# Optimization experiments

Hardware: AMD Instinct MI355X
Metric: run time of the kernel (lower is better)

Reference implementation:

```python
import jax, jax.numpy as jnp
import numpy as np

NUM_GRAPHS = 128
HIDDEN = 256
EPS = 1e-8


def setup_inputs() -> dict:
    key = jax.random.key(0)
    k1, k2, k3, k4, k5, k6, k7 = jax.random.split(key, 7)
    N = 100000
    node_feat = jax.random.normal(k1, (N, HIDDEN), dtype=jnp.float32)
    node_pos = jax.random.normal(k2, (N, 3), dtype=jnp.float32)
    batch = jnp.sort(jax.random.randint(k3, (N,), 0, NUM_GRAPHS))
    # mlp_node_feat: Linear(1, hidden) -> SiLU -> Linear(hidden, hidden)
    W1 = jax.random.normal(k4, (1, HIDDEN), dtype=jnp.float32) * (1.0 / np.sqrt(1.0))
    b1 = jax.random.normal(k5, (HIDDEN,), dtype=jnp.float32) * 0.01
    W2 = jax.random.normal(k6, (HIDDEN, HIDDEN), dtype=jnp.float32) * (1.0 / np.sqrt(HIDDEN))
    b2 = jax.random.normal(k7, (HIDDEN,), dtype=jnp.float32) * 0.01
    return {"node_feat": node_feat, "node_pos": node_pos, "batch": batch,
            "W1": W1, "b1": b1, "W2": W2, "b2": b2}


def _scatter_mean(x, seg, num_segments):
    # sum per segment / count (empty segments -> 0, matching nan_to_num)
    sums = jax.ops.segment_sum(x, seg, num_segments=num_segments)
    counts = jax.ops.segment_sum(jnp.ones((x.shape[0], 1), x.dtype), seg,
                                 num_segments=num_segments)
    return jnp.where(counts > 0, sums / jnp.maximum(counts, 1.0), 0.0)


def reference(node_feat, node_pos, batch, W1, b1, W2, b2):
    # center of each graph, gathered back to nodes
    center = _scatter_mean(node_pos, batch, NUM_GRAPHS)          # [G, 3]
    pos = node_pos - center[batch]                               # [N, 3]
    # safe_norm with keepdim
    scalar = jnp.maximum(jnp.linalg.norm(pos, axis=1, keepdims=True), EPS)  # [N, 1]
    # mlp_node_feat: Linear -> SiLU -> Linear
    h = jax.nn.silu(scalar @ W1 + b1)                            # [N, H]
    return h @ W2 + b2                                           # [N, H]
```

## Files before the change

kernel.cpp:

```cpp
#include <hip/hip_runtime.h>
#include <math.h>

#define HIDDEN   256
#define G_NUM    128
#define TN       1024
#define DS       (1.0f/64.0f)
#define INV_DS   64.0f
#define TM       4
#define TBLOCKS  (TN/TM)
#define CBLOCKS  G_NUM
#define LGRID    2048

typedef float f32x4 __attribute__((ext_vector_type(4)));

__device__ __forceinline__ float readlane_f(float v, int l) {
    union { float f; unsigned u; } a, r;
    a.f = v;
    r.u = __builtin_amdgcn_readlane(a.u, l);
    return r.f;
}

__device__ __forceinline__ float silu_f(float x) {
    return x / (1.f + __expf(-x));
}

__global__ __launch_bounds__(256)
void prep_kernel(const float* __restrict__ pos,
                 const int*   __restrict__ batch,
                 const float* __restrict__ W1,
                 const float* __restrict__ b1,
                 const float* __restrict__ W2,
                 const float* __restrict__ b2,
                 int N,
                 float* __restrict__ U,
                 float* __restrict__ T)
{
    const int bid = blockIdx.x;
    const int tid = threadIdx.x;

    if (bid < TBLOCKS) {
        int k  = tid;
        int l  = tid & 63;
        int m0 = bid * TM;
        float s0 = (float)(m0 + 0) * DS;
        float s1 = (float)(m0 + 1) * DS;
        float s2 = (float)(m0 + 2) * DS;
        float s3 = (float)(m0 + 3) * DS;
        float a0 = 0.f, a1 = 0.f, a2 = 0.f, a3 = 0.f;

        for (int c = 0; c < HIDDEN / 64; ++c) {
            int jb = c * 64;
            float w1 = W1[jb + l];
            float bb = b1[jb + l];
            float h0 = silu_f(fmaf(s0, w1, bb));
            float h1 = silu_f(fmaf(s1, w1, bb));
            float h2 = silu_f(fmaf(s2, w1, bb));
            float h3 = silu_f(fmaf(s3, w1, bb));
            const float* w2p = W2 + (size_t)jb * HIDDEN + k;
            #pragma unroll
            for (int jj = 0; jj < 64; ++jj) {
                float w = w2p[(size_t)jj * HIDDEN];
                a0 = fmaf(readlane_f(h0, jj), w, a0);
                a1 = fmaf(readlane_f(h1, jj), w, a1);
                a2 = fmaf(readlane_f(h2, jj), w, a2);
                a3 = fmaf(readlane_f(h3, jj), w, a3);
            }
        }
        float bv = b2[k];
        T[(size_t)(m0 + 0) * HIDDEN + k] = a0 + bv;
        T[(size_t)(m0 + 1) * HIDDEN + k] = a1 + bv;
        T[(size_t)(m0 + 2) * HIDDEN + k] = a2 + bv;
        T[(size_t)(m0 + 3) * HIDDEN + k] = a3 + bv;
        return;
    }

    int g = bid - TBLOCKS;

    int lo0 = 0, hi0 = N, lo1 = 0, hi1 = N;
    while (lo0 < hi0 || lo1 < hi1) {
        if (lo0 < hi0) { int m = (lo0 + hi0) >> 1; if (batch[m] <  g) lo0 = m + 1; else hi0 = m; }
        if (lo1 < hi1) { int m = (lo1 + hi1) >> 1; if (batch[m] <= g) lo1 = m + 1; else hi1 = m; }
    }
    int start = lo0, end = lo1;
    int cnt = end - start;
    if (cnt <= 0) return;

    float sx = 0.f, sy = 0.f, sz = 0.f;
    for (int n = start + tid; n < end; n += 256) {
        sx += pos[n * 3 + 0];
        sy += pos[n * 3 + 1];
        sz += pos[n * 3 + 2];
    }
    #pragma unroll
    for (int m = 32; m > 0; m >>= 1) {
        sx += __shfl_xor(sx, m, 64);
        sy += __shfl_xor(sy, m, 64);
        sz += __shfl_xor(sz, m, 64);
    }
    __shared__ float cw[3][4];
    __shared__ float ctr[3];
    int w    = tid >> 6;
    int lane = tid & 63;
    if (lane == 0) { cw[0][w] = sx; cw[1][w] = sy; cw[2][w] = sz; }
    __syncthreads();
    if (tid == 0) {
        float inv = 1.f / (float)cnt;
        ctr[0] = (cw[0][0] + cw[0][1] + cw[0][2] + cw[0][3]) * inv;
        ctr[1] = (cw[1][0] + cw[1][1] + cw[1][2] + cw[1][3]) * inv;
        ctr[2] = (cw[2][0] + cw[2][1] + cw[2][2] + cw[2][3]) * inv;
    }
    __syncthreads();
    float cx = ctr[0], cy = ctr[1], cz = ctr[2];

    for (int n = start + tid; n < end; n += 256) {
        float dx = pos[n * 3 + 0] - cx;
        float dy = pos[n * 3 + 1] - cy;
        float dz = pos[n * 3 + 2] - cz;
        float s  = fmaxf(sqrtf(fmaf(dx, dx, fmaf(dy, dy, dz * dz))), 1e-8f);
        U[n] = s * INV_DS;
    }
}

__global__ __launch_bounds__(256)
void lerp_kernel(const float* __restrict__ U,
                 const float* __restrict__ T,
                 float* __restrict__ out, int N)
{
    const int w      = (blockIdx.x << 2) | (threadIdx.x >> 6);
    const int l      = threadIdx.x & 63;
    const int stride = LGRID * 4;

    const f32x4* T4   = (const f32x4*)T;
    f32x4*       out4 = (f32x4*)out;

    int n = w;
    for (; n + stride < N; n += 2 * stride) {
        int n1 = n + stride;
        float u0 = U[n];
        float u1 = U[n1];
        int   i0 = (int)u0; i0 = (i0 < TN - 2) ? i0 : (TN - 2);
        int   i1 = (int)u1; i1 = (i1 < TN - 2) ? i1 : (TN - 2);
        float f0 = u0 - (float)i0;
        float f1 = u1 - (float)i1;
        f32x4 A0 = T4[(size_t)i0       * (HIDDEN / 4) + l];
        f32x4 B0 = T4[(size_t)(i0 + 1) * (HIDDEN / 4) + l];
        f32x4 A1 = T4[(size_t)i1       * (HIDDEN / 4) + l];
        f32x4 B1 = T4[(size_t)(i1 + 1) * (HIDDEN / 4) + l];
        f32x4 o0, o1;
        o0.x = fmaf(f0, B0.x - A0.x, A0.x);
        o0.y = fmaf(f0, B0.y - A0.y, A0.y);
        o0.z = fmaf(f0, B0.z - A0.z, A0.z);
        o0.w = fmaf(f0, B0.w - A0.w, A0.w);
        o1.x = fmaf(f1, B1.x - A1.x, A1.x);
        o1.y = fmaf(f1, B1.y - A1.y, A1.y);
        o1.z = fmaf(f1, B1.z - A1.z, A1.z);
        o1.w = fmaf(f1, B1.w - A1.w, A1.w);
        __builtin_nontemporal_store(o0, &out4[(size_t)n  * (HIDDEN / 4) + l]);
        __builtin_nontemporal_store(o1, &out4[(size_t)n1 * (HIDDEN / 4) + l]);
    }
    for (; n < N; n += stride) {
        float u0 = U[n];
        int   i0 = (int)u0; i0 = (i0 < TN - 2) ? i0 : (TN - 2);
        float f0 = u0 - (float)i0;
        f32x4 A0 = T4[(size_t)i0       * (HIDDEN / 4) + l];
        f32x4 B0 = T4[(size_t)(i0 + 1) * (HIDDEN / 4) + l];
        f32x4 o0;
        o0.x = fmaf(f0, B0.x - A0.x, A0.x);
        o0.y = fmaf(f0, B0.y - A0.y, A0.y);
        o0.z = fmaf(f0, B0.z - A0.z, A0.z);
        o0.w = fmaf(f0, B0.w - A0.w, A0.w);
        __builtin_nontemporal_store(o0, &out4[(size_t)n * (HIDDEN / 4) + l]);
    }
}

extern "C" void kernel_launch(void* const* d_in, const int* in_sizes, int n_in,
                              void* d_out, int out_size, void* d_ws, size_t ws_size,
                              hipStream_t stream) {
    const float* node_pos = (const float*)d_in[1];
    const int*   batch    = (const int*)  d_in[2];
    const float* W1       = (const float*)d_in[3];
    const float* b1       = (const float*)d_in[4];
    const float* W2       = (const float*)d_in[5];
    const float* b2       = (const float*)d_in[6];
    float*       out      = (float*)d_out;

    int N = in_sizes[1] / 3;

    char*  ws = (char*)d_ws;
    float* U  = (float*)ws;
    float* T  = (float*)(ws + (512 << 10));

    prep_kernel<<<TBLOCKS + CBLOCKS, 256, 0, stream>>>(node_pos, batch,
                                                       W1, b1, W2, b2, N, U, T);
    lerp_kernel<<<LGRID, 256, 0, stream>>>(U, T, out, N);
}
```

Measured before the change: 32.02 us.

## Fuse centering and norm into lerp kernel, compute segment bounds by boundary detection

Segment bounds are now found by parallel boundary detection across many blocks instead of a per-graph binary search. The center computation and per-node norm move into the lerp kernel: each of 16 slices per graph recomputes the graph's center and then looks up the table directly. This drops the U intermediate array and its write/read round-trip. The cost is that the center reduction runs 16 times per graph, and load balance now depends on graph sizes.

```diff
diff --git a/kernel.cpp b/kernel.cpp
--- a/kernel.cpp
+++ b/kernel.cpp
@@ -8,8 +8,8 @@
 #define INV_DS   64.0f
 #define TM       4
 #define TBLOCKS  (TN/TM)
-#define CBLOCKS  G_NUM
-#define LGRID    2048
+#define SLICES   16
+#define LGRID    (G_NUM*SLICES)
 
 typedef float f32x4 __attribute__((ext_vector_type(4)));
 
@@ -25,15 +25,14 @@
 }
 
 __global__ __launch_bounds__(256)
-void prep_kernel(const float* __restrict__ pos,
-                 const int*   __restrict__ batch,
-                 const float* __restrict__ W1,
-                 const float* __restrict__ b1,
-                 const float* __restrict__ W2,
-                 const float* __restrict__ b2,
-                 int N,
-                 float* __restrict__ U,
-                 float* __restrict__ T)
+void table_bounds_kernel(const float* __restrict__ W1,
+                         const float* __restrict__ b1,
+                         const float* __restrict__ W2,
+                         const float* __restrict__ b2,
+                         const int*   __restrict__ batch,
+                         int N,
+                         int* __restrict__ bnd0, int* __restrict__ bnd1,
+                         float* __restrict__ T)
 {
     const int bid = blockIdx.x;
     const int tid = threadIdx.x;
@@ -71,18 +70,36 @@
         T[(size_t)(m0 + 1) * HIDDEN + k] = a1 + bv;
         T[(size_t)(m0 + 2) * HIDDEN + k] = a2 + bv;
         T[(size_t)(m0 + 3) * HIDDEN + k] = a3 + bv;
-        return;
-    }
-
-    int g = bid - TBLOCKS;
-
-    int lo0 = 0, hi0 = N, lo1 = 0, hi1 = N;
-    while (lo0 < hi0 || lo1 < hi1) {
-        if (lo0 < hi0) { int m = (lo0 + hi0) >> 1; if (batch[m] <  g) lo0 = m + 1; else hi0 = m; }
-        if (lo1 < hi1) { int m = (lo1 + hi1) >> 1; if (batch[m] <= g) lo1 = m + 1; else hi1 = m; }
-    }
-    int start = lo0, end = lo1;
-    int cnt = end - start;
+    } else {
+        int n = (bid - TBLOCKS) * 256 + tid;
+        if (n < N) {
+            int bn = batch[n];
+            int bp = (n == 0) ? -1 : batch[n - 1];
+            if (bn != bp) {
+                for (int g = bp + 1; g <= bn; ++g) bnd0[g] = n;
+                for (int g = (bp < 0 ? 0 : bp); g < bn; ++g) bnd1[g] = n;
+            }
+            if (n == N - 1) {
+                for (int g = bn; g < G_NUM; ++g) bnd1[g] = N;
+                for (int g = bn + 1; g < G_NUM; ++g) bnd0[g] = N;
+            }
+        }
+    }
+}
+
+__global__ __launch_bounds__(256)
+void center_lerp_kernel(const float* __restrict__ pos,
+                        const int*   __restrict__ bnd0,
+                        const int*   __restrict__ bnd1,
+                        const float* __restrict__ T,
+                        float* __restrict__ out)
+{
+    const int g     = blockIdx.x >> 4;
+    const int slice = blockIdx.x & 15;
+    const int tid   = threadIdx.x;
+    int start = bnd0[g];
+    int end   = bnd1[g];
+    int cnt   = end - start;
     if (cnt <= 0) return;
 
     float sx = 0.f, sy = 0.f, sz = 0.f;
@@ -99,9 +116,9 @@
     }
     __shared__ float cw[3][4];
     __shared__ float ctr[3];
-    int w    = tid >> 6;
-    int lane = tid & 63;
-    if (lane == 0) { cw[0][w] = sx; cw[1][w] = sy; cw[2][w] = sz; }
+    const int w    = tid >> 6;
+    const int l    = tid & 63;
+    if (l == 0) { cw[0][w] = sx; cw[1][w] = sy; cw[2][w] = sz; }
     __syncthreads();
     if (tid == 0) {
         float inv = 1.f / (float)cnt;
@@ -110,34 +127,23 @@
         ctr[2] = (cw[2][0] + cw[2][1] + cw[2][2] + cw[2][3]) * inv;
     }
     __syncthreads();
-    float cx = ctr[0], cy = ctr[1], cz = ctr[2];
-
-    for (int n = start + tid; n < end; n += 256) {
-        float dx = pos[n * 3 + 0] - cx;
-        float dy = pos[n * 3 + 1] - cy;
-        float dz = pos[n * 3 + 2] - cz;
-        float s  = fmaxf(sqrtf(fmaf(dx, dx, fmaf(dy, dy, dz * dz))), 1e-8f);
-        U[n] = s * INV_DS;
-    }
-}
-
-__global__ __launch_bounds__(256)
-void lerp_kernel(const float* __restrict__ U,
-                 const float* __restrict__ T,
-                 float* __restrict__ out, int N)
-{
-    const int w      = (blockIdx.x << 2) | (threadIdx.x >> 6);
-    const int l      = threadIdx.x & 63;
-    const int stride = LGRID * 4;
+    const float cx = ctr[0], cy = ctr[1], cz = ctr[2];
+
+    const int ns = start + (int)(((long long)slice       * cnt) >> 4);
+    const int ne = start + (int)(((long long)(slice + 1) * cnt) >> 4);
 
     const f32x4* T4   = (const f32x4*)T;
     f32x4*       out4 = (f32x4*)out;
 
-    int n = w;
-    for (; n + stride < N; n += 2 * stride) {
-        int n1 = n + stride;
-        float u0 = U[n];
-        float u1 = U[n1];
+    int n = ns + w;
+    for (; n + 4 < ne; n += 8) {
+        int n1 = n + 4;
+        float x0 = pos[n  * 3 + 0], y0 = pos[n  * 3 + 1], z0 = pos[n  * 3 + 2];
+        float x1 = pos[n1 * 3 + 0], y1 = pos[n1 * 3 + 1], z1 = pos[n1 * 3 + 2];
+        float dx0 = x0 - cx, dy0 = y0 - cy, dz0 = z0 - cz;
+        float dx1 = x1 - cx, dy1 = y1 - cy, dz1 = z1 - cz;
+        float u0 = fmaxf(sqrtf(fmaf(dx0, dx0, fmaf(dy0, dy0, dz0 * dz0))), 1e-8f) * INV_DS;
+        float u1 = fmaxf(sqrtf(fmaf(dx1, dx1, fmaf(dy1, dy1, dz1 * dz1))), 1e-8f) * INV_DS;
         int   i0 = (int)u0; i0 = (i0 < TN - 2) ? i0 : (TN - 2);
         int   i1 = (int)u1; i1 = (i1 < TN - 2) ? i1 : (TN - 2);
         float f0 = u0 - (float)i0;
@@ -158,8 +164,10 @@
         __builtin_nontemporal_store(o0, &out4[(size_t)n  * (HIDDEN / 4) + l]);
         __builtin_nontemporal_store(o1, &out4[(size_t)n1 * (HIDDEN / 4) + l]);
     }
-    for (; n < N; n += stride) {
-        float u0 = U[n];
+    for (; n < ne; n += 4) {
+        float x0 = pos[n * 3 + 0], y0 = pos[n * 3 + 1], z0 = pos[n * 3 + 2];
+        float dx0 = x0 - cx, dy0 = y0 - cy, dz0 = z0 - cz;
+        float u0 = fmaxf(sqrtf(fmaf(dx0, dx0, fmaf(dy0, dy0, dz0 * dz0))), 1e-8f) * INV_DS;
         int   i0 = (int)u0; i0 = (i0 < TN - 2) ? i0 : (TN - 2);
         float f0 = u0 - (float)i0;
         f32x4 A0 = T4[(size_t)i0       * (HIDDEN / 4) + l];
@@ -186,11 +194,14 @@
 
     int N = in_sizes[1] / 3;
 
-    char*  ws = (char*)d_ws;
-    float* U  = (float*)ws;
-    float* T  = (float*)(ws + (512 << 10));
-
-    prep_kernel<<<TBLOCKS + CBLOCKS, 256, 0, stream>>>(node_pos, batch,
-                                                       W1, b1, W2, b2, N, U, T);
-    lerp_kernel<<<LGRID, 256, 0, stream>>>(U, T, out, N);
-}
+    char*  ws   = (char*)d_ws;
+    int*   bnd0 = (int*)ws;
+    int*   bnd1 = (int*)(ws + 512);
+    float* T    = (float*)(ws + 4096);
+
+    int boundsBlocks = (N + 255) / 256;
+    table_bounds_kernel<<<TBLOCKS + boundsBlocks, 256, 0, stream>>>(
+        W1, b1, W2, b2, batch, N, bnd0, bnd1, T);
+
+    center_lerp_kernel<<<LGRID, 256, 0, stream>>>(node_pos, bnd0, bnd1, T, out);
+}
```

Result: slower. 34.71 us (+8.4%).
